# Optimization experiments

Measured on AMD Instinct MI355X. Metric: run time of the kernel, lower is better.

## Reference

```python
import jax, jax.numpy as jnp
import numpy as np

N_NODES = 100000
D_IN = 256
D_OUT = 128
N_EDGES = 1600000
KEEP_PROB = 0.5  # tf.nn.dropout(input, 1 - 0.5) -> rate = 0.5


def setup_inputs() -> dict:
    key = jax.random.key(0)
    k_x, k_mask, k_w, k_row, k_col, k_ew = jax.random.split(key, 6)
    x = jax.random.normal(k_x, (N_NODES, D_IN), dtype=jnp.float32)
    # Deterministic scaled dropout keep-mask: Bernoulli(keep)/keep
    u = jax.random.uniform(k_mask, (N_NODES, D_IN), dtype=jnp.float32)
    dropout_mask = (u < KEEP_PROB).astype(jnp.float32) / KEEP_PROB
    kernel = jax.random.normal(k_w, (D_IN, D_OUT), dtype=jnp.float32) * (1.0 / np.sqrt(D_IN))
    edge_row = jax.random.randint(k_row, (N_EDGES,), 0, N_NODES, dtype=jnp.int32)
    edge_col = jax.random.randint(k_col, (N_EDGES,), 0, N_NODES, dtype=jnp.int32)
    edge_weight = jax.random.uniform(k_ew, (N_EDGES,), dtype=jnp.float32)
    return {"x": x, "dropout_mask": dropout_mask, "kernel": kernel,
            "edge_row": edge_row, "edge_col": edge_col, "edge_weight": edge_weight}


def reference(x, dropout_mask, kernel, edge_row, edge_col, edge_weight):
    # dropout (mask already scaled by 1/keep_prob)
    h = x * dropout_mask                      # [N, D_IN]
    # dense projection
    h = h @ kernel                            # [N, D_OUT]
    # sparse (COO) adjacency @ dense: out[r] += w_e * h[c] for each edge (r, c)
    msgs = edge_weight[:, None] * h[edge_col]            # [E, D_OUT]
    agg = jax.ops.segment_sum(msgs, edge_row, num_segments=N_NODES)  # [N, D_OUT]
    # act=True -> relu
    return jax.nn.relu(agg)
```

## Files before the change

kernel.cpp:

```cpp
#include <hip/hip_runtime.h>

constexpr int NN = 100000;
constexpr int DI = 256;
constexpr int DO = 128;
constexpr int NE = 1600000;

constexpr int BROWS = 128;
constexpr int NBK   = (NN + BROWS - 1) / BROWS;
constexpr int TILE  = 8192;
constexpr int CAP   = 2688;

typedef __bf16 bf16x8 __attribute__((ext_vector_type(8)));
typedef float  f32x4  __attribute__((ext_vector_type(4)));

__device__ inline unsigned short f2bf(float f) {
    union { float f; unsigned u; } v; v.f = f;
    return (unsigned short)((v.u + 0x7FFF + ((v.u >> 16) & 1)) >> 16);
}
__device__ inline float bf2f(unsigned u16) {
    union { unsigned u; float f; } v; v.u = u16 << 16;
    return v.f;
}

__global__ __launch_bounds__(256)
void wt_kernel(const float* __restrict__ W, unsigned short* __restrict__ Wt) {
    __shared__ float t[32][33];
    const int tx = threadIdx.x & 31, ty = threadIdx.x >> 5;
    const int k0 = (blockIdx.x >> 2) * 32, n0 = (blockIdx.x & 3) * 32;
#pragma unroll
    for (int i = 0; i < 32; i += 8)
        t[ty + i][tx] = W[(size_t)(k0 + ty + i) * DO + n0 + tx];
    __syncthreads();
#pragma unroll
    for (int i = 0; i < 32; i += 8)
        Wt[(size_t)(n0 + ty + i) * DI + k0 + tx] = f2bf(t[tx][ty + i]);
}

union BF8 { bf16x8 v; unsigned short u[8]; };

__device__ inline bf16x8 mk8(const float4& a, const float4& b,
                             const float4& ma, const float4& mb) {
    BF8 r;
    r.u[0] = f2bf(a.x * ma.x); r.u[1] = f2bf(a.y * ma.y);
    r.u[2] = f2bf(a.z * ma.z); r.u[3] = f2bf(a.w * ma.w);
    r.u[4] = f2bf(b.x * mb.x); r.u[5] = f2bf(b.y * mb.y);
    r.u[6] = f2bf(b.z * mb.z); r.u[7] = f2bf(b.w * mb.w);
    return r.v;
}

__global__ __launch_bounds__(256)
void gemm_kernel(const float* __restrict__ x, const float* __restrict__ mask,
                 const unsigned short* __restrict__ Wt,
                 unsigned short* __restrict__ h) {
    const int tid  = threadIdx.x;
    const int lane = tid & 63;
    const int w    = tid >> 6;
    const int m0   = blockIdx.x * 64;
    const int mw   = w * 16;
    const int l15  = lane & 15;
    const int l4   = lane >> 4;

    const int arow = m0 + mw + l15;
    const size_t rbase = (size_t)(arow < NN ? arow : 0) * DI + l4 * 8;
    const float4* xp = (const float4*)(x + rbase);
    const float4* mp = (const float4*)(mask + rbase);

    f32x4 acc[8];
#pragma unroll
    for (int ct = 0; ct < 8; ++ct) acc[ct] = (f32x4){0.f, 0.f, 0.f, 0.f};

    float4 xr[4], mr[4];
#define LOADA(S)                                                   \
    do {                                                           \
        const int o = (S) * 16;                 \
        xr[0] = xp[o + 0]; xr[1] = xp[o + 1];                      \
        xr[2] = xp[o + 8]; xr[3] = xp[o + 9];                      \
        mr[0] = mp[o + 0]; mr[1] = mp[o + 1];                      \
        mr[2] = mp[o + 8]; mr[3] = mp[o + 9];                      \
    } while (0)

    LOADA(0);
#pragma unroll
    for (int s = 0; s < 4; ++s) {
        const int kc = s * 64;
        const bf16x8 a0 = mk8(xr[0], xr[1], mr[0], mr[1]);
        const bf16x8 a1 = mk8(xr[2], xr[3], mr[2], mr[3]);
        if (s < 3) LOADA(s + 1);
#pragma unroll
        for (int ct = 0; ct < 8; ++ct) {
            const unsigned short* bp =
                Wt + (size_t)(ct * 16 + l15) * DI + kc + l4 * 8;
            const bf16x8 b0 = *(const bf16x8*)(bp);
            const bf16x8 b1 = *(const bf16x8*)(bp + 32);
            acc[ct] = __builtin_amdgcn_mfma_f32_16x16x32_bf16(a0, b0, acc[ct], 0, 0, 0);
            acc[ct] = __builtin_amdgcn_mfma_f32_16x16x32_bf16(a1, b1, acc[ct], 0, 0, 0);
        }
    }
#undef LOADA

#pragma unroll
    for (int ct = 0; ct < 8; ++ct)
#pragma unroll
        for (int reg = 0; reg < 4; ++reg) {
            const int row = m0 + mw + l4 * 4 + reg;
            if (row < NN)
                h[(size_t)row * DO + ct * 16 + l15] = f2bf(acc[ct][reg]);
        }
}

__global__ __launch_bounds__(256)
void part_kernel(const int* __restrict__ erow, const int* __restrict__ ecol,
                 const float* __restrict__ ew, int* __restrict__ bcnt,
                 int2* __restrict__ csr) {
    __shared__ int cnt[NBK];
    __shared__ int base[NBK];
    const int t  = threadIdx.x;
    const int e0 = blockIdx.x * TILE;
    for (int k = t; k < NBK; k += 256) cnt[k] = 0;
    __syncthreads();
    for (int k = 0; k < TILE; k += 256) {
        const int e = e0 + k + t;
        if (e < NE) atomicAdd(&cnt[erow[e] >> 7], 1);
    }
    __syncthreads();
    for (int k = t; k < NBK; k += 256) {
        const int c = cnt[k];
        base[k] = c ? atomicAdd(&bcnt[k], c) : 0;
        cnt[k] = 0;
    }
    __syncthreads();
    for (int k = 0; k < TILE; k += 256) {
        const int e = e0 + k + t;
        if (e < NE) {
            const int row = erow[e];
            const int bk  = row >> 7;
            const int pos = atomicAdd(&cnt[bk], 1);
            int2 v;
            v.x = ((row & 127) << 17) | ecol[e];
            v.y = __float_as_int(ew[e]);
            csr[(size_t)bk * CAP + base[bk] + pos] = v;
        }
    }
}

__global__ __launch_bounds__(512)
void bgather_kernel(const unsigned short* __restrict__ h,
                    const int* __restrict__ bcnt,
                    const int2* __restrict__ csr, float* __restrict__ out) {
    __shared__ int2 se[CAP];
    __shared__ int  s_cnt[BROWS];
    __shared__ int  s_start[BROWS + 1];
    __shared__ int  wtot;
    const int b = blockIdx.x, t = threadIdx.x;
    const int n = bcnt[b];
    const int2* ebase = csr + (size_t)b * CAP;

    if (t < BROWS) s_cnt[t] = 0;
    __syncthreads();
    for (int j = t; j < n; j += 512)
        atomicAdd(&s_cnt[((unsigned)ebase[j].x) >> 17], 1);
    __syncthreads();
    const int lane = t & 63;
    int c = 0;
    if (t < BROWS) c = s_cnt[t];
    int v = c;
#pragma unroll
    for (int off = 1; off < 64; off <<= 1) {
        const int nn = __shfl_up(v, off, 64);
        if (lane >= off) v += nn;
    }
    if (t == 63) wtot = v;
    __syncthreads();
    if (t < BROWS) {
        const int excl = v - c + (t >= 64 ? wtot : 0);
        s_start[t] = excl;
        s_cnt[t]   = excl;
    }
    if (t == 0) s_start[BROWS] = n;
    __syncthreads();
    for (int j = t; j < n; j += 512) {
        const int2 cw  = ebase[j];
        const int  pos = atomicAdd(&s_cnt[((unsigned)cw.x) >> 17], 1);
        se[pos] = cw;
    }
    __syncthreads();

    const int l16 = t & 15, g = t >> 4;
    const int row0 = b * BROWS;
#pragma unroll
    for (int rp = 0; rp < 4; ++rp) {
        const int r  = rp * 32 + g;
        const int gr = row0 + r;
        const int rs = s_start[r], re = s_start[r + 1];
        float acc[8];
#pragma unroll
        for (int i = 0; i < 8; ++i) acc[i] = 0.f;
        int j = rs;
        for (; j + 2 <= re; j += 2) {
            const int2 cw0 = se[j], cw1 = se[j + 1];
            const float w0 = __int_as_float(cw0.y);
            const float w1 = __int_as_float(cw1.y);
            const uint4 q0 = *(const uint4*)(h + (size_t)(cw0.x & 0x1FFFF) * DO + l16 * 8);
            const uint4 q1 = *(const uint4*)(h + (size_t)(cw1.x & 0x1FFFF) * DO + l16 * 8);
            const unsigned* u0 = (const unsigned*)&q0;
            const unsigned* u1 = (const unsigned*)&q1;
#pragma unroll
            for (int i = 0; i < 4; ++i) {
                acc[2 * i + 0] += w0 * bf2f(u0[i] & 0xFFFF) + w1 * bf2f(u1[i] & 0xFFFF);
                acc[2 * i + 1] += w0 * bf2f(u0[i] >> 16)    + w1 * bf2f(u1[i] >> 16);
            }
        }
        if (j < re) {
            const int2 cw = se[j];
            const float w = __int_as_float(cw.y);
            const uint4 q = *(const uint4*)(h + (size_t)(cw.x & 0x1FFFF) * DO + l16 * 8);
            const unsigned* u = (const unsigned*)&q;
#pragma unroll
            for (int i = 0; i < 4; ++i) {
                acc[2 * i + 0] += w * bf2f(u[i] & 0xFFFF);
                acc[2 * i + 1] += w * bf2f(u[i] >> 16);
            }
        }
        if (gr < NN) {
            float* op = out + (size_t)gr * DO + l16 * 8;
            *(float4*)(op + 0) = make_float4(fmaxf(acc[0], 0.f), fmaxf(acc[1], 0.f),
                                             fmaxf(acc[2], 0.f), fmaxf(acc[3], 0.f));
            *(float4*)(op + 4) = make_float4(fmaxf(acc[4], 0.f), fmaxf(acc[5], 0.f),
                                             fmaxf(acc[6], 0.f), fmaxf(acc[7], 0.f));
        }
    }
}

extern "C" void kernel_launch(void* const* d_in, const int* in_sizes, int n_in,
                              void* d_out, int out_size, void* d_ws, size_t ws_size,
                              hipStream_t stream) {
    const float* x    = (const float*)d_in[0];
    const float* mask = (const float*)d_in[1];
    const float* W    = (const float*)d_in[2];
    const int*   erow = (const int*)d_in[3];
    const int*   ecol = (const int*)d_in[4];
    const float* ew   = (const float*)d_in[5];
    float* out = (float*)d_out;

    char* p = (char*)d_ws;
    unsigned short* h  = (unsigned short*)p;  p += (size_t)NN * DO * 2;
    unsigned short* Wt = (unsigned short*)p;  p += (size_t)DO * DI * 2;
    int* bcnt = (int*)p;                      p += 3200;
    int2* csr = (int2*)p;

    hipMemsetAsync(bcnt, 0, NBK * sizeof(int), stream);

    wt_kernel<<<32, 256, 0, stream>>>(W, Wt);
    gemm_kernel<<<(NN + 63) / 64, 256, 0, stream>>>(x, mask, Wt, h);
    part_kernel<<<(NE + TILE - 1) / TILE, 256, 0, stream>>>(erow, ecol, ew,
                                                            bcnt, csr);
    bgather_kernel<<<NBK, 512, 0, stream>>>(h, bcnt, csr, out);
}
```

Before: 397.6 us.

## Stage GEMM A operands through double-buffered LDS via direct global-to-LDS loads

Changes the projection GEMM to fetch x and the dropout mask with global_load_lds DMA into two swizzled LDS buffers. Each buffer is refilled while the other is consumed by the MFMA steps, replacing the previous register-prefetch scheme. The goal is to hide global-load latency for the bandwidth-heavy A-operand reads and cut VGPR pressure. The XOR swizzle is there to avoid LDS bank conflicts. The cost is 64 KB of LDS per block, which may reduce occupancy, plus a dependence on the compiler inserting correct vmcnt waits before LDS reads.

```diff
diff --git a/kernel.cpp b/kernel.cpp
--- a/kernel.cpp
+++ b/kernel.cpp
@@ -48,10 +48,18 @@
     return r.v;
 }
 
+__device__ inline void gload_lds16(const float* g, float* l) {
+    __builtin_amdgcn_global_load_lds(
+        (const __attribute__((address_space(1))) void*)(g),
+        (__attribute__((address_space(3))) void*)(l), 16, 0, 0);
+}
+
 __global__ __launch_bounds__(256)
 void gemm_kernel(const float* __restrict__ x, const float* __restrict__ mask,
                  const unsigned short* __restrict__ Wt,
                  unsigned short* __restrict__ h) {
+    __shared__ float sxA[64][64], smA[64][64];
+    __shared__ float sxB[64][64], smB[64][64];
     const int tid  = threadIdx.x;
     const int lane = tid & 63;
     const int w    = tid >> 6;
@@ -59,52 +67,65 @@
     const int mw   = w * 16;
     const int l15  = lane & 15;
     const int l4   = lane >> 4;
-
-    const int arow = m0 + mw + l15;
-    const size_t rbase = (size_t)(arow < NN ? arow : 0) * DI + l4 * 8;
-    const float4* xp = (const float4*)(x + rbase);
-    const float4* mp = (const float4*)(mask + rbase);
+    const int row  = mw + l15;
+    const int rx   = row & 7;
 
     f32x4 acc[8];
 #pragma unroll
     for (int ct = 0; ct < 8; ++ct) acc[ct] = (f32x4){0.f, 0.f, 0.f, 0.f};
 
-    float4 xr[4], mr[4];
-#define LOADA(S)                                                   \
-    do {                                                           \
-        const int o = (S) * 16;                 \
-        xr[0] = xp[o + 0]; xr[1] = xp[o + 1];                      \
-        xr[2] = xp[o + 8]; xr[3] = xp[o + 9];                      \
-        mr[0] = mp[o + 0]; mr[1] = mp[o + 1];                      \
-        mr[2] = mp[o + 8]; mr[3] = mp[o + 9];                      \
+#define STAGE(SX, SM, K0)                                                  \
+    do {                                                                   \
+        _Pragma("unroll")                                                  \
+        for (int j = 0; j < 4; ++j) {                                      \
+            const int rr = mw + j * 4 + (lane >> 4);                       \
+            const int cs = ((lane & 15) ^ (rr & 7)) * 4;                   \
+            int grow = m0 + rr; if (grow >= NN) grow = NN - 1;             \
+            const size_t go = (size_t)grow * DI + (K0) + cs;               \
+            gload_lds16(x + go,    &SX[mw + j * 4][0]);                    \
+            gload_lds16(mask + go, &SM[mw + j * 4][0]);                    \
+        }                                                                  \
     } while (0)
 
-    LOADA(0);
-#pragma unroll
-    for (int s = 0; s < 4; ++s) {
-        const int kc = s * 64;
-        const bf16x8 a0 = mk8(xr[0], xr[1], mr[0], mr[1]);
-        const bf16x8 a1 = mk8(xr[2], xr[3], mr[2], mr[3]);
-        if (s < 3) LOADA(s + 1);
-#pragma unroll
-        for (int ct = 0; ct < 8; ++ct) {
-            const unsigned short* bp =
-                Wt + (size_t)(ct * 16 + l15) * DI + kc + l4 * 8;
-            const bf16x8 b0 = *(const bf16x8*)(bp);
-            const bf16x8 b1 = *(const bf16x8*)(bp + 32);
-            acc[ct] = __builtin_amdgcn_mfma_f32_16x16x32_bf16(a0, b0, acc[ct], 0, 0, 0);
-            acc[ct] = __builtin_amdgcn_mfma_f32_16x16x32_bf16(a1, b1, acc[ct], 0, 0, 0);
-        }
-    }
-#undef LOADA
+#define STEP(SX, SM, KC)                                                   \
+    do {                                                                   \
+        _Pragma("unroll")                                                  \
+        for (int ks = 0; ks < 2; ++ks) {                                   \
+            const int c0 = ks * 8 + l4 * 2;                                \
+            const float4 xa = *(const float4*)&SX[row][((c0    ) ^ rx)*4]; \
+            const float4 xb = *(const float4*)&SX[row][((c0 + 1) ^ rx)*4]; \
+            const float4 na = *(const float4*)&SM[row][((c0    ) ^ rx)*4]; \
+            const float4 nb = *(const float4*)&SM[row][((c0 + 1) ^ rx)*4]; \
+            const bf16x8 a = mk8(xa, xb, na, nb);                          \
+            _Pragma("unroll")                                              \
+            for (int ct = 0; ct < 8; ++ct) {                               \
+                const bf16x8 b = *(const bf16x8*)(Wt +                     \
+                    (size_t)(ct * 16 + l15) * DI + (KC) + ks * 32 + l4*8); \
+                acc[ct] = __builtin_amdgcn_mfma_f32_16x16x32_bf16(         \
+                    a, b, acc[ct], 0, 0, 0);                               \
+            }                                                              \
+        }                                                                  \
+    } while (0)
+
+    STAGE(sxA, smA, 0);
+    STAGE(sxB, smB, 64);
+    STEP(sxA, smA, 0);
+    STAGE(sxA, smA, 128);
+    STEP(sxB, smB, 64);
+    STAGE(sxB, smB, 192);
+    STEP(sxA, smA, 128);
+    STEP(sxB, smB, 192);
+
+#undef STAGE
+#undef STEP
 
 #pragma unroll
     for (int ct = 0; ct < 8; ++ct)
 #pragma unroll
         for (int reg = 0; reg < 4; ++reg) {
-            const int row = m0 + mw + l4 * 4 + reg;
-            if (row < NN)
-                h[(size_t)row * DO + ct * 16 + l15] = f2bf(acc[ct][reg]);
+            const int r = m0 + mw + l4 * 4 + reg;
+            if (r < NN)
+                h[(size_t)r * DO + ct * 16 + l15] = f2bf(acc[ct][reg]);
         }
 }
 
```

After: 405.5 us. Within noise of the previous version (+2.0%).
